# Optimization experiments

Measured on AMD Instinct MI355X. Metric: run time of the kernel, lower is better.

The kernel has to match this reference:

```python
import jax, jax.numpy as jnp
import numpy as np

B, T, D, H = 4, 2048, 1024, 4
DK = D // H      # head_k_dim = 256
DV = D // H      # head_v_dim = 256
M = DK           # num_slots defaults to head_k_dim
GATE_NORM = 16.0
CLAMP_MIN, CLAMP_MAX = -32.0, 32.0
EPS = 1e-5
ROPE_BASE = 10000.0


def setup_inputs() -> dict:
    key = jax.random.key(0)
    ks = jax.random.split(key, 8)
    sd = 0.02  # stands in for xavier_uniform with gain 2**-2.5
    return {
        "hidden_states": jax.random.normal(ks[0], (B, T, D), jnp.float32),
        "q_w": jax.random.normal(ks[1], (D, D), jnp.float32) * sd,
        "k_w": jax.random.normal(ks[2], (D, D), jnp.float32) * sd,
        "v_w": jax.random.normal(ks[3], (D, D), jnp.float32) * sd,
        "g_w": jax.random.normal(ks[4], (D, D), jnp.float32) * sd,
        "s_w": jax.random.normal(ks[5], (D, H * M), jnp.float32) * sd,
        "sg_w": jax.random.normal(ks[6], (D, H), jnp.float32) * sd,
        "gn_w": jnp.ones((DV,), jnp.float32),
        "o_w": jax.random.normal(ks[7], (D, D), jnp.float32) * sd,
    }


def _rope(x):
    # x: [B, T, H, DK]; non-interleaved (flash-attn style) rotary, full head dim
    half = x.shape[-1] // 2
    inv = 1.0 / (ROPE_BASE ** (jnp.arange(half, dtype=jnp.float32) / half))
    ang = jnp.arange(x.shape[1], dtype=jnp.float32)[:, None] * inv[None, :]  # [T, half]
    cos = jnp.cos(ang)[None, :, None, :]
    sin = jnp.sin(ang)[None, :, None, :]
    x1, x2 = x[..., :half], x[..., half:]
    return jnp.concatenate([x1 * cos - x2 * sin, x2 * cos + x1 * sin], -1)


def _abc(q, k, v, s):
    # ABC linear attention with slot memory (fla chunk_abc semantics, g=None path).
    # q, k: [B,H,T,DK]; v: [B,H,T,DV]; s: [B,H,T,M] (clamped slot logits)
    scale = q.shape[-1] ** -0.5
    z = jax.lax.cumlogsumexp(s, axis=2)                    # running log-normalizer
    s_n = jnp.exp(s - z)                                   # normalized slot write weights
    g = jnp.exp(jnp.concatenate([z[:, :, :1], z[:, :, :-1]], 2) - z)  # per-step decay in (0,1]

    tm = lambda x: jnp.moveaxis(x, 2, 0)                   # time-major for scan

    # stage 1: key memory  hk[B,H,DK,M];  ok_t = scale * q_t @ hk_t
    def step_k(hk, inp):
        q_t, k_t, s_t, g_t = inp
        hk = hk * g_t[:, :, None, :] + k_t[..., None] * s_t[:, :, None, :]
        return hk, jnp.einsum('bhk,bhkm->bhm', q_t, hk)
    hk0 = jnp.zeros(q.shape[:2] + (q.shape[-1], s.shape[-1]), q.dtype)
    _, ok = jax.lax.scan(step_k, hk0, (tm(q * scale), tm(k), tm(s_n), tm(g)))

    qv = jax.nn.softmax(ok, axis=-1)                       # slot read weights, [T,B,H,M]

    # stage 2: value memory  hv[B,H,M,DV];  ov_t = qv_t @ hv_t
    def step_v(hv, inp):
        qv_t, v_t, s_t, g_t = inp
        hv = hv * g_t[..., None] + s_t[..., None] * v_t[:, :, None, :]
        return hv, jnp.einsum('bhm,bhmv->bhv', qv_t, hv)
    hv0 = jnp.zeros(v.shape[:2] + (s.shape[-1], v.shape[-1]), v.dtype)
    _, ov = jax.lax.scan(step_v, hv0, (qv, tm(v), tm(s_n), tm(g)))
    return jnp.moveaxis(ov, 0, 2)                          # [B,H,T,DV]


def reference(hidden_states, q_w, k_w, v_w, g_w, s_w, sg_w, gn_w, o_w):
    x = hidden_states
    q = (x @ q_w).reshape(B, T, H, DK)
    k = (x @ k_w).reshape(B, T, H, DK)
    v = (x @ v_w).reshape(B, T, H, DV).transpose(0, 2, 1, 3)       # [B,H,T,DV]
    q, k = _rope(q), _rope(k)
    q = q.transpose(0, 2, 1, 3)                                    # [B,H,T,DK]
    k = k.transpose(0, 2, 1, 3)

    s = (x @ s_w).reshape(B, T, H, M).transpose(0, 2, 1, 3)        # [B,H,T,M]
    s = jnp.clip(s, CLAMP_MIN, CLAMP_MAX)

    sg = jax.nn.log_sigmoid(x @ sg_w).transpose(0, 2, 1) / GATE_NORM  # [B,H,T]
    k = k * jnp.exp(jnp.cumsum(sg, axis=2))[..., None]

    o = _abc(q, k, v, s).transpose(0, 2, 1, 3)                     # [B,T,H,DV]

    g = (x @ g_w).reshape(B, T, H, DV)
    rms = o * jax.lax.rsqrt(jnp.mean(o * o, axis=-1, keepdims=True) + EPS) * gn_w
    o = (rms * g * jax.nn.sigmoid(g)).reshape(B, T, D)             # RMSNorm + swish gate
    return o @ o_w
```

## Files before the change

### kernel.cpp

```cpp
#include <hip/hip_runtime.h>
#include <hip/hip_bf16.h>
#include <stdint.h>
#include <stddef.h>
#include <math.h>

typedef __bf16 bf8_t __attribute__((ext_vector_type(8)));
typedef __bf16 bf4_t __attribute__((ext_vector_type(4)));
typedef float  f4_t  __attribute__((ext_vector_type(4)));
typedef unsigned int u32;

#define DEV static __device__ __forceinline__

namespace abc {
constexpr int B = 4, T = 2048, D = 1024, H = 4;
constexpr int BT = B * T;
constexpr int CH = 64;
constexpr int NC = T / CH;
constexpr int BH = B * H;
constexpr float SCALE = 0.0625f;
constexpr float GN = 16.0f;
constexpr float EPS = 1e-5f;
}

DEV f4_t mfma16(bf8_t a, bf8_t b, f4_t c) {
  return __builtin_amdgcn_mfma_f32_16x16x32_bf16(a, b, c, 0, 0, 0);
}

DEV void glds16(const void* g, void* l) {
  __builtin_amdgcn_global_load_lds(
      (const __attribute__((address_space(1))) u32*)g,
      (__attribute__((address_space(3))) u32*)l, 16, 0, 0);
}

template<int ROWS>
DEV void stage(const __bf16* __restrict__ g, int S ,
               __bf16* lds, int tid) {
  #pragma unroll
  for (int i = 0; i < ROWS / 64; i++) {
    int p = i * 256 + tid;
    int m = p >> 2;
    int q = (p & 3) ^ (m & 3);
    glds16(g + (size_t)m * S + q * 8, lds + (i * 256 + (tid & ~63)) * 8);
  }
}
DEV bf8_t bfrag(const __bf16* sl, int m, int quad) {
  return *reinterpret_cast<const bf8_t*>(sl + m * 32 + ((quad ^ (m & 3)) << 3));
}

DEV void ring_pre(int s) {
  if (s < 46)       asm volatile("s_waitcnt vmcnt(4)" ::: "memory");
  else if (s == 46) asm volatile("s_waitcnt vmcnt(2)" ::: "memory");
  else              asm volatile("s_waitcnt vmcnt(0)" ::: "memory");
  asm volatile("s_waitcnt lgkmcnt(0)" ::: "memory");
  asm volatile("s_barrier" ::: "memory");
}

__global__ __launch_bounds__(256)
void cvt_x_kernel(const float* __restrict__ x, __bf16* __restrict__ xb)
{
  const int idx = blockIdx.x * 256 + threadIdx.x;
  const float4* src = reinterpret_cast<const float4*>(x);
  float4 a = src[(size_t)idx * 2];
  float4 b = src[(size_t)idx * 2 + 1];
  bf8_t o;
  o[0] = (__bf16)a.x; o[1] = (__bf16)a.y; o[2] = (__bf16)a.z; o[3] = (__bf16)a.w;
  o[4] = (__bf16)b.x; o[5] = (__bf16)b.y; o[6] = (__bf16)b.z; o[7] = (__bf16)b.w;
  reinterpret_cast<bf8_t*>(xb)[idx] = o;
}

__global__ __launch_bounds__(256)
void cvt_w_kernel(const float* __restrict__ w0, const float* __restrict__ w1,
                  const float* __restrict__ w2, const float* __restrict__ w3,
                  const float* __restrict__ w4, const float* __restrict__ w5,
                  __bf16* __restrict__ wt)
{
  const int z = blockIdx.z;
  const float* W = (z == 0) ? w0 : (z == 1) ? w1 : (z == 2) ? w2
                 : (z == 3) ? w3 : (z == 4) ? w4 : w5;
  const int n0 = blockIdx.x * 64, k0 = blockIdx.y * 64;
  __shared__ __bf16 Ts[64][72];
  const int tid = threadIdx.x;
  #pragma unroll
  for (int i = 0; i < 4; i++) {
    int p = tid + 256 * i;
    int row = p >> 4, c4 = p & 15;
    float4 v = *reinterpret_cast<const float4*>(W + (size_t)(k0 + row) * 1024 + n0 + c4 * 4);
    Ts[c4 * 4 + 0][row] = (__bf16)v.x;
    Ts[c4 * 4 + 1][row] = (__bf16)v.y;
    Ts[c4 * 4 + 2][row] = (__bf16)v.z;
    Ts[c4 * 4 + 3][row] = (__bf16)v.w;
  }
  __syncthreads();
  #pragma unroll
  for (int i = 0; i < 2; i++) {
    int p = tid + 256 * i;
    int n = p >> 3, kq = p & 7;
    bf8_t o = *reinterpret_cast<const bf8_t*>(&Ts[n][kq * 8]);
    *reinterpret_cast<bf8_t*>(wt + (size_t)z * 1024 * 1024 + (size_t)(n0 + n) * 1024 + k0 + kq * 8) = o;
  }
}

template<bool OUT_BF16, int NZ>
__global__ __launch_bounds__(256)
void gemm_bt_kernel(const __bf16* __restrict__ A, const __bf16* __restrict__ BtB,
                    void* __restrict__ Cp)
{
  using namespace abc;
  constexpr int K = 1024;
  constexpr int NZC = 8 * NZ;
  const int bflat = blockIdx.x;
  const int xcd = bflat & 7;
  const int j = bflat >> 3;
  const int m_local = j / NZC;
  const int nz = j % NZC;
  const int nt = nz & 7, z = nz >> 3;
  const int m0 = (xcd * 8 + m_local) * 128;
  const int n0 = nt * 128;
  const __bf16* Bt = BtB + (size_t)z * K * 1024;
  __shared__ __bf16 As[128 * 64];
  __shared__ __bf16 Bs[128 * 64];
  const int tid = threadIdx.x;
  const int lane = tid & 63, wvid = tid >> 6;
  const int wr = wvid >> 1, wc = wvid & 1;
  const int quad = lane >> 4, l16 = lane & 15;
  const f4_t fzero = {0.f, 0.f, 0.f, 0.f};
  f4_t acc[4][4];
  #pragma unroll
  for (int i = 0; i < 4; i++)
    #pragma unroll
    for (int j2 = 0; j2 < 4; j2++) acc[i][j2] = fzero;

  const int chunk_row = tid >> 3;
  const int chunk_col = tid & 7;
  for (int k0 = 0; k0 < K; k0 += 64) {
    __syncthreads();
    #pragma unroll
    for (int i = 0; i < 4; i++) {
      glds16(A + (size_t)(m0 + i * 32 + chunk_row) * K + k0 + chunk_col * 8,
             &As[(size_t)(i * 256 + wvid * 64) * 8]);
    }
    #pragma unroll
    for (int i = 0; i < 4; i++) {
      glds16(Bt + (size_t)(n0 + i * 32 + chunk_row) * K + k0 + chunk_col * 8,
             &Bs[(size_t)(i * 256 + wvid * 64) * 8]);
    }
    __syncthreads();
    #pragma unroll
    for (int ks = 0; ks < 2; ks++) {
      bf8_t af[4], bfv[4];
      #pragma unroll
      for (int i = 0; i < 4; i++)
        af[i] = *reinterpret_cast<const bf8_t*>(
            &As[(size_t)(wr * 64 + i * 16 + l16) * 64 + ks * 32 + quad * 8]);
      #pragma unroll
      for (int j2 = 0; j2 < 4; j2++)
        bfv[j2] = *reinterpret_cast<const bf8_t*>(
            &Bs[(size_t)(wc * 64 + j2 * 16 + l16) * 64 + ks * 32 + quad * 8]);
      #pragma unroll
      for (int i = 0; i < 4; i++)
        #pragma unroll
        for (int j2 = 0; j2 < 4; j2++)
          acc[i][j2] = mfma16(af[i], bfv[j2], acc[i][j2]);
    }
  }
  const int crow = m0 + wr * 64, ccol = n0 + wc * 64;
  if (OUT_BF16) {
    __bf16* C = (__bf16*)Cp + (size_t)z * BT * 1024;
    #pragma unroll
    for (int i = 0; i < 4; i++)
      #pragma unroll
      for (int j2 = 0; j2 < 4; j2++)
        #pragma unroll
        for (int r = 0; r < 4; r++)
          C[(size_t)(crow + i * 16 + quad * 4 + r) * 1024 + ccol + j2 * 16 + l16] =
              (__bf16)acc[i][j2][r];
  } else {
    float* C = (float*)Cp;
    #pragma unroll
    for (int i = 0; i < 4; i++)
      #pragma unroll
      for (int j2 = 0; j2 < 4; j2++)
        #pragma unroll
        for (int r = 0; r < 4; r++)
          C[(size_t)(crow + i * 16 + quad * 4 + r) * 1024 + ccol + j2 * 16 + l16] =
              acc[i][j2][r];
  }
}

__global__ __launch_bounds__(256)
void sg_kernel(const float* __restrict__ x, const float* __restrict__ sgw,
               float* __restrict__ sgl)
{
  using namespace abc;
  const int wvid = threadIdx.x >> 6, lane = threadIdx.x & 63;
  const int bt = blockIdx.x * 4 + wvid;
  const float* xr = x + (size_t)bt * 1024;
  float a0 = 0, a1 = 0, a2 = 0, a3 = 0;
  #pragma unroll 4
  for (int u = 0; u < 16; u++) {
    int i = u * 64 + lane;
    float xv = xr[i];
    float4 w = *reinterpret_cast<const float4*>(sgw + (size_t)i * 4);
    a0 += xv * w.x; a1 += xv * w.y; a2 += xv * w.z; a3 += xv * w.w;
  }
  #pragma unroll
  for (int off = 32; off > 0; off >>= 1) {
    a0 += __shfl_down(a0, off);
    a1 += __shfl_down(a1, off);
    a2 += __shfl_down(a2, off);
    a3 += __shfl_down(a3, off);
  }
  if (lane == 0) {
    const int b = bt >> 11, t = bt & (T - 1);
    float r[4] = {a0, a1, a2, a3};
    #pragma unroll
    for (int h = 0; h < 4; h++) {
      float v = r[h];
      float ls = fminf(v, 0.f) - log1pf(expf(-fabsf(v)));
      sgl[(size_t)(b * 4 + h) * T + t] = ls * (1.0f / GN);
    }
  }
}

__global__ __launch_bounds__(256)
void scan_kernel(const float* __restrict__ sgl, float* __restrict__ sgc)
{
  using namespace abc;
  const int bh = blockIdx.x;
  const float* in = sgl + (size_t)bh * T;
  float* out = sgc + (size_t)bh * T;
  __shared__ float part[256];
  const int tid = threadIdx.x;
  float v[8]; float s = 0.f;
  #pragma unroll
  for (int i = 0; i < 8; i++) { v[i] = in[tid * 8 + i]; s += v[i]; }
  part[tid] = s;
  __syncthreads();
  for (int off = 1; off < 256; off <<= 1) {
    float a = (tid >= off) ? part[tid - off] : 0.f;
    __syncthreads();
    part[tid] += a;
    __syncthreads();
  }
  float run = (tid > 0) ? part[tid - 1] : 0.f;
  #pragma unroll
  for (int i = 0; i < 8; i++) { run += v[i]; out[tid * 8 + i] = run; }
}

__global__ __launch_bounds__(256)
void prep_kernel(__bf16* __restrict__ q, __bf16* __restrict__ k,
                 __bf16* __restrict__ s, const float* __restrict__ sgc)
{
  using namespace abc;
  const int bt = blockIdx.x;
  const int b = bt >> 11, t = bt & (T - 1);
  const int tid = threadIdx.x;
  const size_t ro = (size_t)bt * 1024;
  #pragma unroll
  for (int i = 0; i < 2; i++) {
    int p = tid + 256 * i;
    int h = p >> 7, d = p & 127;
    float inv = expf(-(float)d * (9.210340371976184f / 128.0f));
    float ang = (float)t * inv;
    float sn, cs;
    sincosf(ang, &sn, &cs);
    size_t base = ro + (size_t)h * 256 + d;
    float q1 = (float)q[base], q2 = (float)q[base + 128];
    q[base]       = (__bf16)(q1 * cs - q2 * sn);
    q[base + 128] = (__bf16)(q2 * cs + q1 * sn);
    float dec = expf(sgc[(size_t)(b * 4 + h) * T + t]);
    float k1 = (float)k[base], k2 = (float)k[base + 128];
    k[base]       = (__bf16)((k1 * cs - k2 * sn) * dec);
    k[base + 128] = (__bf16)((k2 * cs + k1 * sn) * dec);
  }
  #pragma unroll
  for (int i = 0; i < 4; i++) {
    int e = tid + 256 * i;
    float v = (float)s[ro + e];
    v = fminf(fmaxf(v, -32.f), 32.f);
    s[ro + e] = (__bf16)expf(v);
  }
}

__global__ __launch_bounds__(256)
void transpose_kernel(const __bf16* __restrict__ s0, const __bf16* __restrict__ s1,
                      __bf16* __restrict__ d0, __bf16* __restrict__ d1)
{
  using namespace abc;
  const int c = blockIdx.x, bh = blockIdx.y, z = blockIdx.z;
  const int b = bh >> 2, h = bh & 3;
  const size_t R = (size_t)b * T + (size_t)c * CH;
  const int F = h * 256;
  const __bf16* src = z ? s1 : s0;
  __bf16* dst = (z ? d1 : d0) + ((size_t)bh * NC + c) * (256 * 64);
  __shared__ __bf16 L[256 * 64];
  const int tid = threadIdx.x;
  #pragma unroll
  for (int j = 0; j < 8; j++) {
    int p = tid + 256 * j;
    int t = p >> 5, fc = p & 31;
    bf8_t v = *reinterpret_cast<const bf8_t*>(src + (R + t) * 1024 + F + fc * 8);
    const int sw = ((t >> 3) ^ (fc & 7)) * 8 + (t & 7);
    #pragma unroll
    for (int u = 0; u < 8; u++)
      L[(fc * 8 + u) * 64 + sw] = v[u];
  }
  __syncthreads();
  #pragma unroll
  for (int j = 0; j < 8; j++) {
    int p = tid + 256 * j;
    int f = p >> 3, q = p & 7;
    int phys = q ^ ((f >> 3) & 7);
    bf8_t o = *reinterpret_cast<const bf8_t*>(&L[f * 64 + phys * 8]);
    *reinterpret_cast<bf8_t*>(dst + (size_t)f * 64 + q * 8) = o;
  }
}

__global__ __launch_bounds__(256)
void chunkstate_kernel(const __bf16* __restrict__ KT, const __bf16* __restrict__ VT,
                       const __bf16* __restrict__ AT,
                       __bf16* __restrict__ HKc, __bf16* __restrict__ HVc,
                       float* __restrict__ csA)
{
  using namespace abc;
  const int c = blockIdx.x, bh = blockIdx.y, part = blockIdx.z;
  const size_t TB = ((size_t)bh * NC + c) * (256 * 64);
  const bool isHV = part >= 2;
  const int p2 = part & 1;
  const __bf16* Aop = (isHV ? VT : AT) + TB;
  const __bf16* Bop = (isHV ? AT : KT) + TB;
  const int tid = threadIdx.x;
  if (part == 2) {
    float ssum = 0.f;
    #pragma unroll
    for (int u = 0; u < 8; u++) {
      bf8_t v = *reinterpret_cast<const bf8_t*>(AT + TB + (size_t)tid * 64 + u * 8);
      #pragma unroll
      for (int w = 0; w < 8; w++) ssum += (float)v[w];
    }
    csA[((size_t)bh * NC + c) * 256 + tid] = ssum;
  }
  const int lane = tid & 63, wvid = tid >> 6;
  const int quad = lane >> 4, l16 = lane & 15;
  const int row0 = p2 * 128 + wvid * 32;
  const f4_t fzero = {0.f, 0.f, 0.f, 0.f};
  f4_t acc[2][16];
  #pragma unroll
  for (int a = 0; a < 2; a++)
    #pragma unroll
    for (int ct = 0; ct < 16; ct++) acc[a][ct] = fzero;
  #pragma unroll
  for (int ks = 0; ks < 2; ks++) {
    bf8_t af0 = *reinterpret_cast<const bf8_t*>(Aop + (size_t)(row0 + l16) * 64 + ks * 32 + quad * 8);
    bf8_t af1 = *reinterpret_cast<const bf8_t*>(Aop + (size_t)(row0 + 16 + l16) * 64 + ks * 32 + quad * 8);
    #pragma unroll
    for (int ct = 0; ct < 16; ct++) {
      bf8_t bv = *reinterpret_cast<const bf8_t*>(Bop + (size_t)(ct * 16 + l16) * 64 + ks * 32 + quad * 8);
      acc[0][ct] = mfma16(af0, bv, acc[0][ct]);
      acc[1][ct] = mfma16(af1, bv, acc[1][ct]);
    }
  }
  __bf16* out = (isHV ? HVc : HKc) + ((size_t)bh * NC + c) * 65536;
  #pragma unroll
  for (int rt = 0; rt < 2; rt++)
    #pragma unroll
    for (int ct = 0; ct < 16; ct++)
      #pragma unroll
      for (int r = 0; r < 4; r++)
        out[(size_t)(row0 + rt * 16 + quad * 4 + r) * 256 + ct * 16 + l16] =
            (__bf16)acc[rt][ct][r];
}

__global__ __launch_bounds__(256)
void prefix_state_kernel(__bf16* __restrict__ HKc, __bf16* __restrict__ HVc)
{
  using namespace abc;
  const int bh = blockIdx.y;
  __bf16* base = (blockIdx.z ? HVc : HKc) + (size_t)bh * NC * 65536;
  const int e = (blockIdx.x * 256 + threadIdx.x) * 8;
  float run[8];
  #pragma unroll
  for (int u = 0; u < 8; u++) run[u] = 0.f;
  #pragma unroll 4
  for (int c = 0; c < NC; c++) {
    __bf16* p = base + (size_t)c * 65536 + e;
    bf8_t v = *reinterpret_cast<const bf8_t*>(p);
    bf8_t o;
    #pragma unroll
    for (int u = 0; u < 8; u++) { o[u] = (__bf16)run[u]; run[u] += (float)v[u]; }
    *reinterpret_cast<bf8_t*>(p) = o;
  }
}

__global__ __launch_bounds__(256)
void prefix_csa_kernel(float* __restrict__ csA)
{
  using namespace abc;
  const int bh = blockIdx.x, m = threadIdx.x;
  float run = 0.f;
  for (int c = 0; c < NC; c++) {
    float* p = csA + ((size_t)bh * NC + c) * 256 + m;
    float v = *p; *p = run; run += v;
  }
}

__global__ __launch_bounds__(256)
void attn_kernel(const __bf16* __restrict__ qg, const __bf16* __restrict__ kg,
                 const __bf16* __restrict__ ag, const __bf16* __restrict__ gg,
                 const __bf16* __restrict__ ATp, const __bf16* __restrict__ VTp,
                 const __bf16* __restrict__ HKp, const __bf16* __restrict__ HVp,
                 const float* __restrict__ Zp, const float* __restrict__ gnw,
                 __bf16* __restrict__ yout)
{
  using namespace abc;
  const int c = blockIdx.x, bh = blockIdx.y;
  const int b = bh >> 2, h = bh & 3;
  const size_t R = (size_t)b * T + (size_t)c * CH;
  const int F = h * 256;
  const int tid = threadIdx.x;
  const int lane = tid & 63, wvid = tid >> 6;
  const int quad = lane >> 4, l16 = lane & 15;

  __shared__ __bf16 ST[4][4096];
  __shared__ __bf16 Ws[64][264];
  __shared__ __bf16 S1s[64][72];
  __shared__ float zs[256];
  __shared__ float gns[256];

  const __bf16* atb = ATp + ((size_t)bh * NC + c) * (256 * 64);
  const __bf16* vtb = VTp + ((size_t)bh * NC + c) * (256 * 64);
  const __bf16* hkb = HKp + ((size_t)bh * NC + c) * 65536;
  const __bf16* hvb = HVp + ((size_t)bh * NC + c) * 65536;
  const __bf16* kbase = kg + R * 1024 + F;
  const __bf16* abase = ag + R * 1024 + F;

  zs[tid] = Zp[((size_t)bh * NC + c) * 256 + tid];
  gns[tid] = gnw[tid];
  __syncthreads();

  const __bf16* qrow = qg + (R + wvid * 16 + l16) * 1024 + F;
  bf8_t aq[8];
  #pragma unroll
  for (int ks = 0; ks < 8; ks++)
    aq[ks] = *reinterpret_cast<const bf8_t*>(qrow + ks * 32 + quad * 8);

  const f4_t fzero = {0.f, 0.f, 0.f, 0.f};

  auto issue = [&](int s) {
    if (s >= 48) return;
    __bf16* buf = &ST[s & 3][0];
    if (s < 4) {
      stage<64>(kbase + (2 * s) * 32, 1024, buf, tid);
      stage<64>(kbase + (2 * s + 1) * 32, 1024, buf + 2048, tid);
    } else if (s < 8) {
      int j = s - 4, iks = j >> 1, rh = j & 1;
      stage<128>(atb + rh * 128 * 64 + iks * 32, 64, buf, tid);
    } else if (s < 24) {
      int j = s - 8, ks = j >> 1, rh = j & 1;
      stage<128>(hkb + (size_t)rh * 128 * 256 + ks * 32, 256, buf, tid);
    } else if (s < 28) {
      int j = s - 24;
      stage<64>(abase + (2 * j) * 32, 1024, buf, tid);
      stage<64>(abase + (2 * j + 1) * 32, 1024, buf + 2048, tid);
    } else if (s < 44) {
      int j = s - 28, ks = j >> 1, rh = j & 1;
      stage<128>(hvb + (size_t)rh * 128 * 256 + ks * 32, 256, buf, tid);
    } else {
      int j = s - 44, iks = j >> 1, rh = j & 1;
      stage<128>(vtb + rh * 128 * 64 + iks * 32, 64, buf, tid);
    }
  };

  issue(0); issue(1); issue(2);

  f4_t s1a[4];
  #pragma unroll
  for (int it = 0; it < 4; it++) s1a[it] = fzero;
  #pragma unroll
  for (int j = 0; j < 4; j++) {
    ring_pre(j);
    issue(j + 3);
    const __bf16* sl = &ST[j & 3][0];
    #pragma unroll
    for (int ks2 = 0; ks2 < 2; ks2++) {
      bf8_t a = aq[2 * j + ks2];
      const __bf16* sb = sl + ks2 * 2048;
      #pragma unroll
      for (int it = 0; it < 4; it++)
        s1a[it] = mfma16(a, bfrag(sb, it * 16 + l16, quad), s1a[it]);
    }
  }
  #pragma unroll
  for (int it = 0; it < 4; it++)
    #pragma unroll
    for (int r = 0; r < 4; r++) {
      int tl = wvid * 16 + quad * 4 + r;
      int il = it * 16 + l16;
      S1s[tl][il] = (il <= tl) ? (__bf16)s1a[it][r] : (__bf16)0.0f;
    }

  f4_t aok[16], acum[16];
  #pragma unroll
  for (int mt = 0; mt < 16; mt++) { aok[mt] = fzero; acum[mt] = fzero; }
  #pragma unroll
  for (int j = 0; j < 4; j++) {
    int s = 4 + j, iks = j >> 1, rh = j & 1;
    ring_pre(s);
    issue(s + 3);
    const __bf16* sl = &ST[s & 3][0];
    bf8_t s1f = *reinterpret_cast<const bf8_t*>(&S1s[wvid * 16 + l16][iks * 32 + quad * 8]);
    bf8_t lf;
    #pragma unroll
    for (int u = 0; u < 8; u++)
      lf[u] = (iks * 32 + quad * 8 + u <= wvid * 16 + l16) ? (__bf16)1.0f : (__bf16)0.0f;
    #pragma unroll
    for (int m8 = 0; m8 < 8; m8++) {
      bf8_t bfa = bfrag(sl, m8 * 16 + l16, quad);
      aok[rh * 8 + m8]  = mfma16(s1f, bfa, aok[rh * 8 + m8]);
      acum[rh * 8 + m8] = mfma16(lf,  bfa, acum[rh * 8 + m8]);
    }
  }

  #pragma unroll
  for (int j = 0; j < 16; j++) {
    int s = 8 + j, ks = j >> 1, rh = j & 1;
    ring_pre(s);
    issue(s + 3);
    const __bf16* sl = &ST[s & 3][0];
    #pragma unroll
    for (int m8 = 0; m8 < 8; m8++) {
      bf8_t bv = bfrag(sl, m8 * 16 + l16, quad);
      aok[rh * 8 + m8] = mfma16(aq[ks], bv, aok[rh * 8 + m8]);
    }
  }

  #pragma unroll
  for (int r = 0; r < 4; r++) {
    float ovv[16], sa[16];
    float mx = -3.0e38f;
    #pragma unroll
    for (int mt = 0; mt < 16; mt++) {
      sa[mt] = zs[mt * 16 + l16] + acum[mt][r];
      ovv[mt] = SCALE * aok[mt][r] / sa[mt];
      mx = fmaxf(mx, ovv[mt]);
    }
    #pragma unroll
    for (int off = 1; off < 16; off <<= 1) mx = fmaxf(mx, __shfl_xor(mx, off));
    float se = 0.f;
    #pragma unroll
    for (int mt = 0; mt < 16; mt++) { ovv[mt] = __expf(ovv[mt] - mx); se += ovv[mt]; }
    #pragma unroll
    for (int off = 1; off < 16; off <<= 1) se += __shfl_xor(se, off);
    float inv = 1.0f / se;
    int tl = wvid * 16 + quad * 4 + r;
    #pragma unroll
    for (int mt = 0; mt < 16; mt++)
      Ws[tl][mt * 16 + l16] = (__bf16)(ovv[mt] * inv / sa[mt]);
  }

  f4_t pacc[4];
  #pragma unroll
  for (int it = 0; it < 4; it++) pacc[it] = fzero;
  #pragma unroll
  for (int j = 0; j < 4; j++) {
    int s = 24 + j;
    ring_pre(s);
    issue(s + 3);
    const __bf16* sl = &ST[s & 3][0];
    #pragma unroll
    for (int ks2 = 0; ks2 < 2; ks2++) {
      int ks = 2 * j + ks2;
      bf8_t wf = *reinterpret_cast<const bf8_t*>(&Ws[wvid * 16 + l16][ks * 32 + quad * 8]);
      const __bf16* sb = sl + ks2 * 2048;
      #pragma unroll
      for (int it = 0; it < 4; it++)
        pacc[it] = mfma16(wf, bfrag(sb, it * 16 + l16, quad), pacc[it]);
    }
  }
  #pragma unroll
  for (int it = 0; it < 4; it++)
    #pragma unroll
    for (int r = 0; r < 4; r++) {
      int tl = wvid * 16 + quad * 4 + r;
      int il = it * 16 + l16;
      S1s[tl][il] = (il <= tl) ? (__bf16)pacc[it][r] : (__bf16)0.0f;
    }

  f4_t oacc[16];
  #pragma unroll
  for (int vt = 0; vt < 16; vt++) oacc[vt] = fzero;
  #pragma unroll
  for (int j = 0; j < 16; j++) {
    int s = 28 + j, ks = j >> 1, rh = j & 1;
    ring_pre(s);
    issue(s + 3);
    const __bf16* sl = &ST[s & 3][0];
    bf8_t wf = *reinterpret_cast<const bf8_t*>(&Ws[wvid * 16 + l16][ks * 32 + quad * 8]);
    #pragma unroll
    for (int v8 = 0; v8 < 8; v8++) {
      bf8_t bv = bfrag(sl, v8 * 16 + l16, quad);
      oacc[rh * 8 + v8] = mfma16(wf, bv, oacc[rh * 8 + v8]);
    }
  }

  #pragma unroll
  for (int j = 0; j < 4; j++) {
    int s = 44 + j, iks = j >> 1, rh = j & 1;
    ring_pre(s);
    issue(s + 3);
    const __bf16* sl = &ST[s & 3][0];
    bf8_t pf = *reinterpret_cast<const bf8_t*>(&S1s[wvid * 16 + l16][iks * 32 + quad * 8]);
    #pragma unroll
    for (int v8 = 0; v8 < 8; v8++) {
      bf8_t bvt = bfrag(sl, v8 * 16 + l16, quad);
      oacc[rh * 8 + v8] = mfma16(pf, bvt, oacc[rh * 8 + v8]);
    }
  }

  #pragma unroll
  for (int r = 0; r < 4; r++) {
    float ss = 0.f;
    #pragma unroll
    for (int vt = 0; vt < 16; vt++) ss += oacc[vt][r] * oacc[vt][r];
    #pragma unroll
    for (int off = 1; off < 16; off <<= 1) ss += __shfl_xor(ss, off);
    float rinv = rsqrtf(ss * (1.0f / 256.0f) + EPS);
    int tl = wvid * 16 + quad * 4 + r;
    const __bf16* grow = gg + (R + tl) * 1024 + F;
    __bf16* yrow = yout + (R + tl) * 1024 + F;
    #pragma unroll
    for (int vt = 0; vt < 16; vt++) {
      int v = vt * 16 + l16;
      float gvl = (float)grow[v];
      float yv = oacc[vt][r] * rinv * gns[v] * gvl / (1.0f + __expf(-gvl));
      yrow[v] = (__bf16)yv;
    }
  }
}

extern "C" void kernel_launch(void* const* d_in, const int* in_sizes, int n_in,
                              void* d_out, int out_size, void* d_ws, size_t ws_size,
                              hipStream_t stream) {
  using namespace abc;
  (void)in_sizes; (void)n_in; (void)out_size; (void)ws_size;
  const float* x    = (const float*)d_in[0];
  const float* q_w  = (const float*)d_in[1];
  const float* k_w  = (const float*)d_in[2];
  const float* v_w  = (const float*)d_in[3];
  const float* g_w  = (const float*)d_in[4];
  const float* s_w  = (const float*)d_in[5];
  const float* sg_w = (const float*)d_in[6];
  const float* gn_w = (const float*)d_in[7];
  const float* o_w  = (const float*)d_in[8];
  float* out = (float*)d_out;

  char* ws = (char*)d_ws;
  const size_t PROJ = (size_t)BT * 1024;
  __bf16* proj = (__bf16*)ws;
  __bf16* q_bf = proj + 0 * PROJ;
  __bf16* k_bf = proj + 1 * PROJ;
  __bf16* v_bf = proj + 2 * PROJ;
  __bf16* g_bf = proj + 3 * PROJ;
  __bf16* a_bf = proj + 4 * PROJ;
  __bf16* xb   = proj + 5 * PROJ;
  float* sgl = (float*)(ws + (size_t)96 * 1024 * 1024);
  float* sgc = sgl + (size_t)BH * T;
  float* csA = sgc + (size_t)BH * T;
  __bf16* HKc = (__bf16*)(ws + (size_t)97 * 1024 * 1024);
  __bf16* HVc = HKc + (size_t)BH * NC * 65536;
  __bf16* wt  = (__bf16*)(ws + (size_t)225 * 1024 * 1024);
  __bf16* KT  = (__bf16*)(ws + (size_t)237 * 1024 * 1024);
  __bf16* VT  = xb;
  __bf16* AT  = v_bf;
  __bf16* y_bf = KT;

  dim3 blk(256);
  cvt_w_kernel<<<dim3(16, 16, 6), blk, 0, stream>>>(q_w, k_w, v_w, g_w, s_w, o_w, wt);
  cvt_x_kernel<<<dim3(BT * 1024 / (256 * 8)), blk, 0, stream>>>(x, xb);
  gemm_bt_kernel<true, 5><<<dim3(64 * 8 * 5), blk, 0, stream>>>(xb, wt, proj);
  sg_kernel<<<dim3(BT / 4), blk, 0, stream>>>(x, sg_w, sgl);
  scan_kernel<<<dim3(BH), blk, 0, stream>>>(sgl, sgc);
  prep_kernel<<<dim3(BT), blk, 0, stream>>>(q_bf, k_bf, a_bf, sgc);
  transpose_kernel<<<dim3(NC, BH, 2), blk, 0, stream>>>(k_bf, v_bf, KT, VT);
  transpose_kernel<<<dim3(NC, BH, 1), blk, 0, stream>>>(a_bf, a_bf, AT, AT);
  chunkstate_kernel<<<dim3(NC, BH, 4), blk, 0, stream>>>(KT, VT, AT, HKc, HVc, csA);
  prefix_state_kernel<<<dim3(32, BH, 2), blk, 0, stream>>>(HKc, HVc);
  prefix_csa_kernel<<<dim3(BH), blk, 0, stream>>>(csA);
  attn_kernel<<<dim3(NC, BH), blk, 0, stream>>>(
      q_bf, k_bf, a_bf, g_bf, AT, VT, HKc, HVc, csA, gn_w, y_bf);
  gemm_bt_kernel<false, 1><<<dim3(64 * 8), blk, 0, stream>>>(
      y_bf, wt + (size_t)5 * 1024 * 1024, out);
}
```

Baseline: 513.4 us.

## Store transposed V/A and chunk states in pre-swizzled LDS slice layout

```diff
diff --git a/kernel.cpp b/kernel.cpp
--- a/kernel.cpp
+++ b/kernel.cpp
@@ -30,6 +30,21 @@
   __builtin_amdgcn_global_load_lds(
       (const __attribute__((address_space(1))) u32*)g,
       (__attribute__((address_space(3))) u32*)l, 16, 0, 0);
+}
+
+DEV __bf16* slice_addr(__bf16* base, int row, int cg ) {
+  return base + (((cg >> 2) * 2 + (row >> 7)) * 4096
+               + ((((row & 127) << 2) | ((cg & 3) ^ (row & 3))) * 8));
+}
+DEV const __bf16* slice_addr(const __bf16* base, int row, int cg) {
+  return base + (((cg >> 2) * 2 + (row >> 7)) * 4096
+               + ((((row & 127) << 2) | ((cg & 3) ^ (row & 3))) * 8));
+}
+
+DEV void stage_lin(const __bf16* __restrict__ g, __bf16* lds, int tid) {
+  #pragma unroll
+  for (int i = 0; i < 2; i++)
+    glds16(g + (size_t)(i * 256 + tid) * 8, lds + (i * 256 + (tid & ~63)) * 8);
 }
 
 template<int ROWS>
@@ -282,6 +297,7 @@
   }
 }
 
+template<bool NEW0, bool NEW1>
 __global__ __launch_bounds__(256)
 void transpose_kernel(const __bf16* __restrict__ s0, const __bf16* __restrict__ s1,
                       __bf16* __restrict__ d0, __bf16* __restrict__ d1)
@@ -293,6 +309,7 @@
   const int F = h * 256;
   const __bf16* src = z ? s1 : s0;
   __bf16* dst = (z ? d1 : d0) + ((size_t)bh * NC + c) * (256 * 64);
+  const bool NEWL = z ? NEW1 : NEW0;
   __shared__ __bf16 L[256 * 64];
   const int tid = threadIdx.x;
   #pragma unroll
@@ -312,7 +329,9 @@
     int f = p >> 3, q = p & 7;
     int phys = q ^ ((f >> 3) & 7);
     bf8_t o = *reinterpret_cast<const bf8_t*>(&L[f * 64 + phys * 8]);
-    *reinterpret_cast<bf8_t*>(dst + (size_t)f * 64 + q * 8) = o;
+    __bf16* daddr = NEWL ? slice_addr(dst, f, q)
+                         : dst + (size_t)f * 64 + q * 8;
+    *reinterpret_cast<bf8_t*>(daddr) = o;
   }
 }
 
@@ -334,7 +353,7 @@
     float ssum = 0.f;
     #pragma unroll
     for (int u = 0; u < 8; u++) {
-      bf8_t v = *reinterpret_cast<const bf8_t*>(AT + TB + (size_t)tid * 64 + u * 8);
+      bf8_t v = *reinterpret_cast<const bf8_t*>(slice_addr(AT + TB, tid, u));
       #pragma unroll
       for (int w = 0; w < 8; w++) ssum += (float)v[w];
     }
@@ -351,11 +370,16 @@
     for (int ct = 0; ct < 16; ct++) acc[a][ct] = fzero;
   #pragma unroll
   for (int ks = 0; ks < 2; ks++) {
-    bf8_t af0 = *reinterpret_cast<const bf8_t*>(Aop + (size_t)(row0 + l16) * 64 + ks * 32 + quad * 8);
-    bf8_t af1 = *reinterpret_cast<const bf8_t*>(Aop + (size_t)(row0 + 16 + l16) * 64 + ks * 32 + quad * 8);
+    const int cg = ks * 4 + quad;
+    bf8_t af0 = *reinterpret_cast<const bf8_t*>(slice_addr(Aop, row0 + l16, cg));
+    bf8_t af1 = *reinterpret_cast<const bf8_t*>(slice_addr(Aop, row0 + 16 + l16, cg));
     #pragma unroll
     for (int ct = 0; ct < 16; ct++) {
-      bf8_t bv = *reinterpret_cast<const bf8_t*>(Bop + (size_t)(ct * 16 + l16) * 64 + ks * 32 + quad * 8);
+      bf8_t bv;
+      if (isHV)
+        bv = *reinterpret_cast<const bf8_t*>(slice_addr(Bop, ct * 16 + l16, cg));
+      else
+        bv = *reinterpret_cast<const bf8_t*>(Bop + (size_t)(ct * 16 + l16) * 64 + ks * 32 + quad * 8);
       acc[0][ct] = mfma16(af0, bv, acc[0][ct]);
       acc[1][ct] = mfma16(af1, bv, acc[1][ct]);
     }
@@ -366,9 +390,11 @@
     #pragma unroll
     for (int ct = 0; ct < 16; ct++)
       #pragma unroll
-      for (int r = 0; r < 4; r++)
-        out[(size_t)(row0 + rt * 16 + quad * 4 + r) * 256 + ct * 16 + l16] =
-            (__bf16)acc[rt][ct][r];
+      for (int r = 0; r < 4; r++) {
+        const int mg = row0 + rt * 16 + quad * 4 + r;
+        const int n  = ct * 16 + l16;
+        *(slice_addr(out, mg, n >> 3) + (n & 7)) = (__bf16)acc[rt][ct][r];
+      }
 }
 
 __global__ __launch_bounds__(256)
@@ -453,21 +479,17 @@
       stage<64>(kbase + (2 * s) * 32, 1024, buf, tid);
       stage<64>(kbase + (2 * s + 1) * 32, 1024, buf + 2048, tid);
     } else if (s < 8) {
-      int j = s - 4, iks = j >> 1, rh = j & 1;
-      stage<128>(atb + rh * 128 * 64 + iks * 32, 64, buf, tid);
+      stage_lin(atb + (s - 4) * 4096, buf, tid);
     } else if (s < 24) {
-      int j = s - 8, ks = j >> 1, rh = j & 1;
-      stage<128>(hkb + (size_t)rh * 128 * 256 + ks * 32, 256, buf, tid);
+      stage_lin(hkb + (s - 8) * 4096, buf, tid);
     } else if (s < 28) {
       int j = s - 24;
       stage<64>(abase + (2 * j) * 32, 1024, buf, tid);
       stage<64>(abase + (2 * j + 1) * 32, 1024, buf + 2048, tid);
     } else if (s < 44) {
-      int j = s - 28, ks = j >> 1, rh = j & 1;
-      stage<128>(hvb + (size_t)rh * 128 * 256 + ks * 32, 256, buf, tid);
+      stage_lin(hvb + (s - 28) * 4096, buf, tid);
     } else {
-      int j = s - 44, iks = j >> 1, rh = j & 1;
-      stage<128>(vtb + rh * 128 * 64 + iks * 32, 64, buf, tid);
+      stage_lin(vtb + (s - 44) * 4096, buf, tid);
     }
   };
 
@@ -681,8 +703,8 @@
   sg_kernel<<<dim3(BT / 4), blk, 0, stream>>>(x, sg_w, sgl);
   scan_kernel<<<dim3(BH), blk, 0, stream>>>(sgl, sgc);
   prep_kernel<<<dim3(BT), blk, 0, stream>>>(q_bf, k_bf, a_bf, sgc);
-  transpose_kernel<<<dim3(NC, BH, 2), blk, 0, stream>>>(k_bf, v_bf, KT, VT);
-  transpose_kernel<<<dim3(NC, BH, 1), blk, 0, stream>>>(a_bf, a_bf, AT, AT);
+  transpose_kernel<false, true><<<dim3(NC, BH, 2), blk, 0, stream>>>(k_bf, v_bf, KT, VT);
+  transpose_kernel<true, true><<<dim3(NC, BH, 1), blk, 0, stream>>>(a_bf, a_bf, AT, AT);
   chunkstate_kernel<<<dim3(NC, BH, 4), blk, 0, stream>>>(KT, VT, AT, HKc, HVc, csA);
   prefix_state_kernel<<<dim3(32, BH, 2), blk, 0, stream>>>(HKc, HVc);
   prefix_csa_kernel<<<dim3(BH), blk, 0, stream>>>(csA);
```

Result: faster. 499.6 us (-2.7%).
